# Kernel optimization log

Measured on AMD Instinct MI355X. Metric: run time of the kernel, lower is better.

## Reference

```python
import jax, jax.numpy as jnp
import numpy as np

EPS = 1e-5


def sage_conv(x, src, dst, Wl, Wr, b, n):
    # PyG SAGEConv: out_i = W_l * mean_{j in N(i)} x_j + W_r * x_i + b
    agg = jax.ops.segment_sum(x[src], dst, num_segments=n)  # [N, d]
    deg = jax.ops.segment_sum(jnp.ones_like(src, dtype=x.dtype), dst, num_segments=n)
    agg = agg / jnp.maximum(deg, 1.0)[:, None]
    return agg @ Wl + x @ Wr + b


def setup_inputs() -> dict:
    key = jax.random.key(0)
    ks = jax.random.split(key, 12)
    N, E, D_IN, D_H, D_OUT = 50000, 600000, 128, 128, 64
    x = jax.random.normal(ks[0], (N, D_IN), dtype=jnp.float32)
    edge_index = jax.random.randint(ks[1], (2, E), 0, N, dtype=jnp.int64)
    s_in = 1.0 / np.sqrt(D_IN)
    s_h = 1.0 / np.sqrt(D_H)
    return {
        "x": x,
        "edge_index": edge_index,
        "Wl0": jax.random.normal(ks[2], (D_IN, D_H), jnp.float32) * s_in,
        "Wr0": jax.random.normal(ks[3], (D_IN, D_H), jnp.float32) * s_in,
        "b0": jnp.zeros((D_H,), jnp.float32),
        "Wl1": jax.random.normal(ks[4], (D_H, D_H), jnp.float32) * s_h,
        "Wr1": jax.random.normal(ks[5], (D_H, D_H), jnp.float32) * s_h,
        "b1": jnp.zeros((D_H,), jnp.float32),
        "Wl2": jax.random.normal(ks[6], (D_H, D_OUT), jnp.float32) * s_h,
        "Wr2": jax.random.normal(ks[7], (D_H, D_OUT), jnp.float32) * s_h,
        "b2": jnp.zeros((D_OUT,), jnp.float32),
        "gamma": jnp.ones((D_H,), jnp.float32),
        "beta": jnp.zeros((D_H,), jnp.float32),
    }


def reference(x, edge_index, Wl0, Wr0, b0, Wl1, Wr1, b1, Wl2, Wr2, b2, gamma, beta):
    n = x.shape[0]
    src, dst = edge_index[0], edge_index[1]
    residual = x  # in_channels == hidden_channels -> no residual_transform
    # layer 0: conv + relu (+ dropout as identity in eval)
    h = jax.nn.relu(sage_conv(x, src, dst, Wl0, Wr0, b0, n))
    # middle layer: conv + BN(batch stats) + relu + residual
    h = sage_conv(h, src, dst, Wl1, Wr1, b1, n)
    mu = jnp.mean(h, axis=0)
    var = jnp.var(h, axis=0)  # biased, as in torch BN normalization
    h = (h - mu) * jax.lax.rsqrt(var + EPS) * gamma + beta
    h = jax.nn.relu(h) + residual
    # output layer
    h = sage_conv(h, src, dst, Wl2, Wr2, b2, n)
    return jax.nn.log_softmax(h, axis=-1)
```

## Files before the change

kernel.cpp:

```cpp
#include <hip/hip_runtime.h>
#include <hip/hip_bf16.h>


#define WS_EPS 1e-5f

typedef unsigned short ushort_t;
typedef unsigned int uint_t;
typedef ushort_t ushort8 __attribute__((ext_vector_type(8)));
typedef short short8 __attribute__((ext_vector_type(8)));
typedef float f32x4 __attribute__((ext_vector_type(4)));

__device__ __forceinline__ float bf2f(ushort_t u) {
    return __uint_as_float(((uint_t)u) << 16);
}
__device__ __forceinline__ ushort_t f2bf(float f) {
    uint_t u = __float_as_uint(f);
    u = (u + 0x7fffu + ((u >> 16) & 1u)) >> 16;
    return (ushort_t)u;
}

__global__ __launch_bounds__(256) void k_deg(const int* __restrict__ ei,
                                             int* __restrict__ deg, int E) {
    int e = blockIdx.x * 256 + threadIdx.x;
    if (e < E) atomicAdd(&deg[ei[E + e]], 1);
}

constexpr int SCHUNK = 4096;

__global__ __launch_bounds__(256) void k_scan_part(const int* __restrict__ deg,
                                                   int* __restrict__ bsum, int n) {
    int t = threadIdx.x;
    int base = blockIdx.x * SCHUNK + t * 16;
    int s = 0;
#pragma unroll
    for (int j = 0; j < 16; ++j) {
        int i = base + j;
        if (i < n) s += deg[i];
    }
#pragma unroll
    for (int d = 1; d < 64; d <<= 1) s += __shfl_xor(s, d);
    __shared__ int wt[4];
    if ((t & 63) == 0) wt[t >> 6] = s;
    __syncthreads();
    if (t == 0) bsum[blockIdx.x] = wt[0] + wt[1] + wt[2] + wt[3];
}

__global__ __launch_bounds__(64) void k_scan_bsum(const int* __restrict__ bsum,
                                                  int* __restrict__ boff,
                                                  int* __restrict__ off_n, int nb) {
    int lane = threadIdx.x;
    int carry = 0;
    for (int base = 0; base < nb; base += 64) {
        int t = base + lane;
        int v = (t < nb) ? bsum[t] : 0;
        int x = v;
#pragma unroll
        for (int d = 1; d < 64; d <<= 1) {
            int y = __shfl_up(x, d);
            if (lane >= d) x += y;
        }
        if (t < nb) boff[t] = carry + x - v;
        carry += __shfl(x, 63);
    }
    if (lane == 0) *off_n = carry;
}

__global__ __launch_bounds__(256) void k_scan_apply(const int* __restrict__ deg,
                                                    const int* __restrict__ boff,
                                                    int* __restrict__ off, int n) {
    int t = threadIdx.x;
    int lane = t & 63, wid = t >> 6;
    int base = blockIdx.x * SCHUNK + t * 16;
    int v[16];
    int s = 0;
#pragma unroll
    for (int j = 0; j < 16; ++j) {
        int i = base + j;
        v[j] = (i < n) ? deg[i] : 0;
        s += v[j];
    }
    int x = s;
#pragma unroll
    for (int d = 1; d < 64; d <<= 1) {
        int y = __shfl_up(x, d);
        if (lane >= d) x += y;
    }
    __shared__ int wtot[4];
    if (lane == 63) wtot[wid] = x;
    __syncthreads();
    int woff = 0;
    for (int wj = 0; wj < wid; ++wj) woff += wtot[wj];
    int run = boff[blockIdx.x] + woff + x - s;
#pragma unroll
    for (int j = 0; j < 16; ++j) {
        int i = base + j;
        if (i < n) off[i] = run;
        run += v[j];
    }
}

__global__ __launch_bounds__(256) void k_scatter(const int* __restrict__ ei,
                                                 const int* __restrict__ off,
                                                 int* __restrict__ cur,
                                                 int* __restrict__ csr, int E) {
    int e = blockIdx.x * 256 + threadIdx.x;
    if (e < E) {
        int d = ei[E + e];
        int s = ei[e];
        int p = atomicAdd(&cur[d], 1);
        csr[off[d] + p] = s;
    }
}

__global__ __launch_bounds__(256) void k_prep(const float* __restrict__ x,
                                              ushort_t* __restrict__ xb, int total2,
                                              int nb_cvt,
                                              const float* __restrict__ Wl0,
                                              const float* __restrict__ Wr0,
                                              const float* __restrict__ Wl1,
                                              const float* __restrict__ Wr1,
                                              const float* __restrict__ Wl2,
                                              const float* __restrict__ Wr2,
                                              ushort_t* __restrict__ wts) {
    int b = blockIdx.x;
    if (b < nb_cvt) {
        int i = b * 256 + threadIdx.x;
        if (i >= total2) return;
        float2 v = *(const float2*)&x[(size_t)i * 2];
        uint_t p = (uint_t)f2bf(v.x) | ((uint_t)f2bf(v.y) << 16);
        *(uint_t*)&xb[(size_t)i * 2] = p;
        return;
    }
    int id = (b - nb_cvt) * 256 + threadIdx.x;
    if (id >= 81920) return;
    const float* W;
    int rel, nout, base;
    if (id < 65536) {
        int m = id >> 14;
        rel = id & 16383;
        nout = 128;
        base = m << 14;
        W = (m == 0) ? Wl0 : (m == 1) ? Wr0 : (m == 2) ? Wl1 : Wr1;
    } else {
        int m = (id - 65536) >> 13;
        rel = (id - 65536) & 8191;
        nout = 64;
        base = 65536 + (m << 13);
        W = (m == 0) ? Wl2 : Wr2;
    }
    int c = rel >> 7;
    int k = rel & 127;
    wts[base + rel] = f2bf(W[(size_t)k * nout + c]);
}

template <int EPI>
__global__ __launch_bounds__(256) void k_fgemm(const ushort_t* __restrict__ X1,
                                               const ushort_t* __restrict__ W1,
                                               const ushort_t* __restrict__ X2,
                                               const ushort_t* __restrict__ W2,
                                               const float* __restrict__ bias,
                                               void* __restrict__ outv,
                                               float* __restrict__ stats, int n) {
    constexpr int NOUT = 128, BM = 128, K = 128, LDK = 136;
    constexpr int WM = 64, WN = 64, FM = 4, FN = 4;

    __shared__ ushort_t Xs[BM * LDK];
    __shared__ ushort_t Ws[NOUT * LDK];

    const int t = threadIdx.x;
    const int row0 = blockIdx.x * BM;
    const int lane = t & 63;
    const int wid = t >> 6;
    const int wr = wid >> 1, wc = wid & 1;
    const int r16 = lane & 15, kb = lane >> 4;

    f32x4 acc[FM][FN];
#pragma unroll
    for (int i = 0; i < FM; ++i)
#pragma unroll
        for (int j = 0; j < FN; ++j) acc[i][j] = (f32x4)0.f;

#pragma unroll
    for (int ph = 0; ph < 2; ++ph) {
        const ushort_t* Xp = ph ? X2 : X1;
        const ushort_t* Wp = ph ? W2 : W1;
        if (ph) __syncthreads();
#pragma unroll
        for (int u = 0; u < 8; ++u) {
            int f = u * 256 + t;
            int r = f >> 4, seg = f & 15;
            int gr = row0 + r;
            ushort8 v = (ushort8)0;
            if (gr < n) v = *(const ushort8*)&Xp[(size_t)gr * K + seg * 8];
            *(ushort8*)&Xs[r * LDK + seg * 8] = v;
        }
#pragma unroll
        for (int u = 0; u < 8; ++u) {
            int f = u * 256 + t;
            int r = f >> 4, seg = f & 15;
            *(ushort8*)&Ws[r * LDK + seg * 8] = *(const ushort8*)&Wp[(size_t)r * K + seg * 8];
        }
        __syncthreads();
#pragma unroll
        for (int ks = 0; ks < 4; ++ks) {
            short8 a[FM], b[FN];
#pragma unroll
            for (int fm = 0; fm < FM; ++fm)
                a[fm] = *(const short8*)&Xs[(wr * WM + fm * 16 + r16) * LDK + ks * 32 + kb * 8];
#pragma unroll
            for (int fn = 0; fn < FN; ++fn)
                b[fn] = *(const short8*)&Ws[(wc * WN + fn * 16 + r16) * LDK + ks * 32 + kb * 8];
#pragma unroll
            for (int fm = 0; fm < FM; ++fm)
#pragma unroll
                for (int fn = 0; fn < FN; ++fn)
                    acc[fm][fn] = __builtin_amdgcn_mfma_f32_16x16x32_bf16(a[fm], b[fn], acc[fm][fn], 0, 0, 0);
        }
    }

    if constexpr (EPI == 2) {
#pragma unroll
        for (int fm = 0; fm < FM; ++fm) {
#pragma unroll
            for (int r = 0; r < 4; ++r) {
                int row = row0 + wr * WM + fm * 16 + kb * 4 + r;
                if (row >= n) continue;
#pragma unroll
                for (int fn = 0; fn < FN; ++fn) {
                    int col = wc * WN + fn * 16 + r16;
                    float v = acc[fm][fn][r] + bias[col];
                    ((ushort_t*)outv)[(size_t)row * NOUT + col] = f2bf(fmaxf(v, 0.f));
                }
            }
        }
    } else {
        float s[FN], q[FN];
#pragma unroll
        for (int fn = 0; fn < FN; ++fn) { s[fn] = 0.f; q[fn] = 0.f; }
#pragma unroll
        for (int fm = 0; fm < FM; ++fm) {
#pragma unroll
            for (int r = 0; r < 4; ++r) {
                int row = row0 + wr * WM + fm * 16 + kb * 4 + r;
                if (row >= n) continue;
#pragma unroll
                for (int fn = 0; fn < FN; ++fn) {
                    int col = wc * WN + fn * 16 + r16;
                    float v = acc[fm][fn][r] + bias[col];
                    ((float*)outv)[(size_t)row * NOUT + col] = v;
                    s[fn] += v;
                    q[fn] += v * v;
                }
            }
        }
#pragma unroll
        for (int fn = 0; fn < FN; ++fn) {
            s[fn] += __shfl_xor(s[fn], 16);
            s[fn] += __shfl_xor(s[fn], 32);
            q[fn] += __shfl_xor(q[fn], 16);
            q[fn] += __shfl_xor(q[fn], 32);
        }
        if (kb == 0) {
#pragma unroll
            for (int fn = 0; fn < FN; ++fn) {
                int col = wc * WN + fn * 16 + r16;
                atomicAdd(&stats[col], s[fn]);
                atomicAdd(&stats[128 + col], q[fn]);
            }
        }
    }
}

template <int EPI>
__global__ __launch_bounds__(256) void k_mgemm64(const ushort_t* __restrict__ X,
                                                 const ushort_t* __restrict__ WT,
                                                 const ushort_t* __restrict__ AGG,
                                                 const float* __restrict__ bias,
                                                 void* __restrict__ outv, int n) {
    constexpr int NOUT = 64, BM = 128, K = 128, LDK = 136;
    constexpr int WM = 32, WN = 64, FM = 2, FN = 4;

    __shared__ ushort_t Xs[BM * LDK];
    __shared__ ushort_t Ws[NOUT * LDK];

    const int t = threadIdx.x;
    const int row0 = blockIdx.x * BM;

#pragma unroll
    for (int u = 0; u < 8; ++u) {
        int f = u * 256 + t;
        int r = f >> 4, seg = f & 15;
        int gr = row0 + r;
        ushort8 v = (ushort8)0;
        if (gr < n) v = *(const ushort8*)&X[(size_t)gr * K + seg * 8];
        *(ushort8*)&Xs[r * LDK + seg * 8] = v;
    }
#pragma unroll
    for (int u = 0; u < 4; ++u) {
        int f = u * 256 + t;
        int r = f >> 4, seg = f & 15;
        *(ushort8*)&Ws[r * LDK + seg * 8] = *(const ushort8*)&WT[(size_t)r * K + seg * 8];
    }
    __syncthreads();

    const int lane = t & 63;
    const int wid = t >> 6;
    const int r16 = lane & 15, kb = lane >> 4;

    f32x4 acc[FM][FN];
#pragma unroll
    for (int i = 0; i < FM; ++i)
#pragma unroll
        for (int j = 0; j < FN; ++j) acc[i][j] = (f32x4)0.f;

#pragma unroll
    for (int ks = 0; ks < 4; ++ks) {
        short8 a[FM], b[FN];
#pragma unroll
        for (int fm = 0; fm < FM; ++fm)
            a[fm] = *(const short8*)&Xs[(wid * WM + fm * 16 + r16) * LDK + ks * 32 + kb * 8];
#pragma unroll
        for (int fn = 0; fn < FN; ++fn)
            b[fn] = *(const short8*)&Ws[(fn * 16 + r16) * LDK + ks * 32 + kb * 8];
#pragma unroll
        for (int fm = 0; fm < FM; ++fm)
#pragma unroll
            for (int fn = 0; fn < FN; ++fn)
                acc[fm][fn] = __builtin_amdgcn_mfma_f32_16x16x32_bf16(a[fm], b[fn], acc[fm][fn], 0, 0, 0);
    }

    if constexpr (EPI == 3) {
        float* outp = (float*)outv;
#pragma unroll
        for (int fm = 0; fm < FM; ++fm) {
#pragma unroll
            for (int r = 0; r < 4; ++r) {
                int row = row0 + wid * WM + fm * 16 + kb * 4 + r;
                bool ok = (row < n);
                float vv[FN];
#pragma unroll
                for (int fn = 0; fn < FN; ++fn) {
                    int col = fn * 16 + r16;
                    vv[fn] = ok ? (acc[fm][fn][r] + bf2f(AGG[(size_t)row * NOUT + col]) + bias[col])
                                : 0.f;
                }
                float m = fmaxf(fmaxf(vv[0], vv[1]), fmaxf(vv[2], vv[3]));
#pragma unroll
                for (int d = 1; d < 16; d <<= 1) m = fmaxf(m, __shfl_xor(m, d));
                float e = expf(vv[0] - m) + expf(vv[1] - m) + expf(vv[2] - m) + expf(vv[3] - m);
#pragma unroll
                for (int d = 1; d < 16; d <<= 1) e += __shfl_xor(e, d);
                float lg = m + logf(e);
                if (ok) {
#pragma unroll
                    for (int fn = 0; fn < FN; ++fn)
                        outp[(size_t)row * NOUT + fn * 16 + r16] = vv[fn] - lg;
                }
            }
        }
    } else {
#pragma unroll
        for (int fm = 0; fm < FM; ++fm) {
#pragma unroll
            for (int r = 0; r < 4; ++r) {
                int row = row0 + wid * WM + fm * 16 + kb * 4 + r;
                if (row >= n) continue;
#pragma unroll
                for (int fn = 0; fn < FN; ++fn) {
                    int col = fn * 16 + r16;
                    ((ushort_t*)outv)[(size_t)row * NOUT + col] = f2bf(acc[fm][fn][r]);
                }
            }
        }
    }
}

template <int D>
__global__ __launch_bounds__(256) void k_segmean_bf(const ushort_t* __restrict__ U,
                                                    const int* __restrict__ off,
                                                    const int* __restrict__ srcs,
                                                    ushort_t* __restrict__ out,
                                                    int n) {
    int node = blockIdx.x * 8 + (threadIdx.x >> 5);
    int sub = threadIdx.x & 31;
    if (node >= n) return;
    int beg = off[node], end = off[node + 1];
    constexpr int CPL = D / 32;
    float a0 = 0.f, a1 = 0.f, a2 = 0.f, a3 = 0.f;
    int i = beg;
    for (; i + 8 <= end; i += 8) {
        int sv[8];
#pragma unroll
        for (int u = 0; u < 8; ++u) sv[u] = srcs[i + u];
#pragma unroll
        for (int u = 0; u < 8; ++u) {
            if (CPL == 4) {
                uint2 v = *(const uint2*)&U[(size_t)sv[u] * D + sub * 4];
                a0 += __uint_as_float(v.x << 16);
                a1 += __uint_as_float(v.x & 0xffff0000u);
                a2 += __uint_as_float(v.y << 16);
                a3 += __uint_as_float(v.y & 0xffff0000u);
            } else {
                uint_t v = *(const uint_t*)&U[(size_t)sv[u] * D + sub * 2];
                a0 += __uint_as_float(v << 16);
                a1 += __uint_as_float(v & 0xffff0000u);
            }
        }
    }
    for (; i + 4 <= end; i += 4) {
        int sv[4];
#pragma unroll
        for (int u = 0; u < 4; ++u) sv[u] = srcs[i + u];
#pragma unroll
        for (int u = 0; u < 4; ++u) {
            if (CPL == 4) {
                uint2 v = *(const uint2*)&U[(size_t)sv[u] * D + sub * 4];
                a0 += __uint_as_float(v.x << 16);
                a1 += __uint_as_float(v.x & 0xffff0000u);
                a2 += __uint_as_float(v.y << 16);
                a3 += __uint_as_float(v.y & 0xffff0000u);
            } else {
                uint_t v = *(const uint_t*)&U[(size_t)sv[u] * D + sub * 2];
                a0 += __uint_as_float(v << 16);
                a1 += __uint_as_float(v & 0xffff0000u);
            }
        }
    }
    for (; i < end; ++i) {
        int s = srcs[i];
        if (CPL == 4) {
            uint2 v = *(const uint2*)&U[(size_t)s * D + sub * 4];
            a0 += __uint_as_float(v.x << 16);
            a1 += __uint_as_float(v.x & 0xffff0000u);
            a2 += __uint_as_float(v.y << 16);
            a3 += __uint_as_float(v.y & 0xffff0000u);
        } else {
            uint_t v = *(const uint_t*)&U[(size_t)s * D + sub * 2];
            a0 += __uint_as_float(v << 16);
            a1 += __uint_as_float(v & 0xffff0000u);
        }
    }
    int d = end - beg;
    float inv = 1.f / (float)(d > 1 ? d : 1);
    if (CPL == 4) {
        uint2 p;
        p.x = (uint_t)f2bf(a0 * inv) | ((uint_t)f2bf(a1 * inv) << 16);
        p.y = (uint_t)f2bf(a2 * inv) | ((uint_t)f2bf(a3 * inv) << 16);
        *(uint2*)&out[(size_t)node * D + sub * 4] = p;
    } else {
        uint_t p = (uint_t)f2bf(a0 * inv) | ((uint_t)f2bf(a1 * inv) << 16);
        *(uint_t*)&out[(size_t)node * D + sub * 2] = p;
    }
}

__global__ __launch_bounds__(256) void k_bnapply(const float* __restrict__ P,
                                                 const float* __restrict__ X,
                                                 const float* __restrict__ stats,
                                                 const float* __restrict__ gamma,
                                                 const float* __restrict__ beta,
                                                 ushort_t* __restrict__ H, int n) {
    int i = blockIdx.x * 256 + threadIdx.x;
    if (i >= n * 64) return;
    int nd = i >> 6;
    int c = (i & 63) << 1;
    float inv_n = 1.f / (float)n;
    float mu0 = stats[c] * inv_n, mu1 = stats[c + 1] * inv_n;
    float v0 = stats[128 + c] * inv_n - mu0 * mu0;
    float v1 = stats[128 + c + 1] * inv_n - mu1 * mu1;
    float s0 = rsqrtf(v0 + WS_EPS) * gamma[c];
    float s1 = rsqrtf(v1 + WS_EPS) * gamma[c + 1];
    float2 p = *(const float2*)&P[(size_t)nd * 128 + c];
    float2 xr = *(const float2*)&X[(size_t)nd * 128 + c];
    float h0 = fmaxf((p.x - mu0) * s0 + beta[c], 0.f) + xr.x;
    float h1 = fmaxf((p.y - mu1) * s1 + beta[c + 1], 0.f) + xr.y;
    uint_t pk = (uint_t)f2bf(h0) | ((uint_t)f2bf(h1) << 16);
    *(uint_t*)&H[(size_t)nd * 128 + c] = pk;
}

extern "C" void kernel_launch(void* const* d_in, const int* in_sizes, int n_in,
                              void* d_out, int out_size, void* d_ws, size_t ws_size,
                              hipStream_t stream) {
    const float* x     = (const float*)d_in[0];
    const int*   ei    = (const int*)d_in[1];
    const float* Wl0   = (const float*)d_in[2];
    const float* Wr0   = (const float*)d_in[3];
    const float* b0    = (const float*)d_in[4];
    const float* Wl1   = (const float*)d_in[5];
    const float* Wr1   = (const float*)d_in[6];
    const float* b1    = (const float*)d_in[7];
    const float* Wl2   = (const float*)d_in[8];
    const float* Wr2   = (const float*)d_in[9];
    const float* b2    = (const float*)d_in[10];
    const float* gamma = (const float*)d_in[11];
    const float* beta  = (const float*)d_in[12];

    const int n = in_sizes[0] / 128;
    const int E = in_sizes[1] / 2;
    const int nb_scan = (n + SCHUNK - 1) / SCHUNK;

    char* w = (char*)d_ws;
    auto alloc = [&](size_t bytes) -> void* {
        void* p = (void*)w;
        w += (bytes + 255) & ~(size_t)255;
        return p;
    };
    int*      deg   = (int*)alloc((size_t)n * 4);
    int*      cur   = (int*)alloc((size_t)n * 4);
    float*    stats = (float*)alloc(256 * 4);
    size_t    zbytes = (size_t)((char*)w - (char*)deg);
    int*      off   = (int*)alloc(((size_t)n + 1) * 4);
    int*      csr   = (int*)alloc((size_t)E * 4);
    int*      bsum  = (int*)alloc(256 * 4);
    int*      boff  = (int*)alloc(256 * 4);
    ushort_t* wts   = (ushort_t*)alloc((size_t)81920 * 2);
    ushort_t* xb    = (ushort_t*)alloc((size_t)n * 128 * 2);
    ushort_t* H     = (ushort_t*)alloc((size_t)n * 128 * 2);
    float*    P     = (float*)alloc((size_t)n * 128 * 4);
    ushort_t* slabB = (ushort_t*)alloc((size_t)n * 128 * 2);

    ushort_t* WtL0 = wts;
    ushort_t* WtR0 = wts + 16384;
    ushort_t* WtL1 = wts + 32768;
    ushort_t* WtR1 = wts + 49152;
    ushort_t* WtL2 = wts + 65536;
    ushort_t* WtR2 = wts + 73728;

    ushort_t* M   = slabB;
    ushort_t* A64 = slabB;
    ushort_t* B64 = slabB + (size_t)n * 64;

    hipMemsetAsync(deg, 0, zbytes, stream);

    const int eb = (E + 255) / 256;
    k_deg<<<eb, 256, 0, stream>>>(ei, deg, E);
    k_scan_part<<<nb_scan, 256, 0, stream>>>(deg, bsum, n);
    k_scan_bsum<<<1, 64, 0, stream>>>(bsum, boff, off + n, nb_scan);
    k_scan_apply<<<nb_scan, 256, 0, stream>>>(deg, boff, off, n);
    k_scatter<<<eb, 256, 0, stream>>>(ei, off, cur, csr, E);

    const int nb_cvt = (n * 64 + 255) / 256;
    k_prep<<<nb_cvt + 320, 256, 0, stream>>>(x, xb, n * 64, nb_cvt,
                                             Wl0, Wr0, Wl1, Wr1, Wl2, Wr2, wts);

    const int gb = (n + 127) / 128;
    const int smb = (n + 7) / 8;

    k_segmean_bf<128><<<smb, 256, 0, stream>>>(xb, off, csr, M, n);
    k_fgemm<2><<<gb, 256, 0, stream>>>(xb, WtR0, M, WtL0, b0, H, nullptr, n);

    k_segmean_bf<128><<<smb, 256, 0, stream>>>(H, off, csr, M, n);
    k_fgemm<1><<<gb, 256, 0, stream>>>(H, WtR1, M, WtL1, b1, P, stats, n);
    k_bnapply<<<(n * 64 + 255) / 256, 256, 0, stream>>>(P, x, stats, gamma, beta, H, n);

    k_mgemm64<0><<<gb, 256, 0, stream>>>(H, WtL2, nullptr, nullptr, A64, n);
    k_segmean_bf<64><<<smb, 256, 0, stream>>>(A64, off, csr, B64, n);
    k_mgemm64<3><<<gb, 256, 0, stream>>>(H, WtR2, B64, b2, (float*)d_out, n);
}
```

Baseline: 233.4 us.

## Halve GEMM row tiles, read weights from global, prefetch second operand, block-reduce BN stats

```diff
diff --git a/kernel.cpp b/kernel.cpp
--- a/kernel.cpp
+++ b/kernel.cpp
@@ -154,18 +154,18 @@
 }
 
 template <int EPI>
-__global__ __launch_bounds__(256) void k_fgemm(const ushort_t* __restrict__ X1,
-                                               const ushort_t* __restrict__ W1,
-                                               const ushort_t* __restrict__ X2,
-                                               const ushort_t* __restrict__ W2,
-                                               const float* __restrict__ bias,
-                                               void* __restrict__ outv,
-                                               float* __restrict__ stats, int n) {
-    constexpr int NOUT = 128, BM = 128, K = 128, LDK = 136;
-    constexpr int WM = 64, WN = 64, FM = 4, FN = 4;
-
-    __shared__ ushort_t Xs[BM * LDK];
-    __shared__ ushort_t Ws[NOUT * LDK];
+__global__ __launch_bounds__(256, 4) void k_fgemm(const ushort_t* __restrict__ X1,
+                                                  const ushort_t* __restrict__ W1,
+                                                  const ushort_t* __restrict__ X2,
+                                                  const ushort_t* __restrict__ W2,
+                                                  const float* __restrict__ bias,
+                                                  void* __restrict__ outv,
+                                                  float* __restrict__ stats, int n) {
+    constexpr int NOUT = 128, K = 128, BM = 64, LDK = 136;
+    constexpr int FM = 2, FN = 4;
+
+    __shared__ ushort_t Xs[2][BM * LDK];
+    __shared__ float sred[256];
 
     const int t = threadIdx.x;
     const int row0 = blockIdx.x * BM;
@@ -173,6 +173,26 @@
     const int wid = t >> 6;
     const int wr = wid >> 1, wc = wid & 1;
     const int r16 = lane & 15, kb = lane >> 4;
+    const int tr = t >> 4, seg = t & 15;
+
+    if (EPI == 1) sred[t] = 0.f;
+
+    ushort8 g[4];
+#pragma unroll
+    for (int u = 0; u < 4; ++u) {
+        int gr = row0 + u * 16 + tr;
+        g[u] = (gr < n) ? *(const ushort8*)&X1[(size_t)gr * K + seg * 8] : (ushort8)0;
+    }
+#pragma unroll
+    for (int u = 0; u < 4; ++u)
+        *(ushort8*)&Xs[0][(u * 16 + tr) * LDK + seg * 8] = g[u];
+    __syncthreads();
+
+#pragma unroll
+    for (int u = 0; u < 4; ++u) {
+        int gr = row0 + u * 16 + tr;
+        g[u] = (gr < n) ? *(const ushort8*)&X2[(size_t)gr * K + seg * 8] : (ushort8)0;
+    }
 
     f32x4 acc[FM][FN];
 #pragma unroll
@@ -181,41 +201,40 @@
         for (int j = 0; j < FN; ++j) acc[i][j] = (f32x4)0.f;
 
 #pragma unroll
-    for (int ph = 0; ph < 2; ++ph) {
-        const ushort_t* Xp = ph ? X2 : X1;
-        const ushort_t* Wp = ph ? W2 : W1;
-        if (ph) __syncthreads();
-#pragma unroll
-        for (int u = 0; u < 8; ++u) {
-            int f = u * 256 + t;
-            int r = f >> 4, seg = f & 15;
-            int gr = row0 + r;
-            ushort8 v = (ushort8)0;
-            if (gr < n) v = *(const ushort8*)&Xp[(size_t)gr * K + seg * 8];
-            *(ushort8*)&Xs[r * LDK + seg * 8] = v;
-        }
-#pragma unroll
-        for (int u = 0; u < 8; ++u) {
-            int f = u * 256 + t;
-            int r = f >> 4, seg = f & 15;
-            *(ushort8*)&Ws[r * LDK + seg * 8] = *(const ushort8*)&Wp[(size_t)r * K + seg * 8];
-        }
-        __syncthreads();
-#pragma unroll
-        for (int ks = 0; ks < 4; ++ks) {
-            short8 a[FM], b[FN];
-#pragma unroll
-            for (int fm = 0; fm < FM; ++fm)
-                a[fm] = *(const short8*)&Xs[(wr * WM + fm * 16 + r16) * LDK + ks * 32 + kb * 8];
+    for (int ks = 0; ks < 4; ++ks) {
+        short8 a[FM], b[FN];
+#pragma unroll
+        for (int fm = 0; fm < FM; ++fm)
+            a[fm] = *(const short8*)&Xs[0][(wr * 32 + fm * 16 + r16) * LDK + ks * 32 + kb * 8];
+#pragma unroll
+        for (int fn = 0; fn < FN; ++fn)
+            b[fn] = *(const short8*)&W1[(size_t)(wc * 64 + fn * 16 + r16) * K + ks * 32 + kb * 8];
+#pragma unroll
+        for (int fm = 0; fm < FM; ++fm)
 #pragma unroll
             for (int fn = 0; fn < FN; ++fn)
-                b[fn] = *(const short8*)&Ws[(wc * WN + fn * 16 + r16) * LDK + ks * 32 + kb * 8];
-#pragma unroll
-            for (int fm = 0; fm < FM; ++fm)
-#pragma unroll
-                for (int fn = 0; fn < FN; ++fn)
-                    acc[fm][fn] = __builtin_amdgcn_mfma_f32_16x16x32_bf16(a[fm], b[fn], acc[fm][fn], 0, 0, 0);
-        }
+                acc[fm][fn] = __builtin_amdgcn_mfma_f32_16x16x32_bf16(a[fm], b[fn], acc[fm][fn], 0, 0, 0);
+    }
+
+#pragma unroll
+    for (int u = 0; u < 4; ++u)
+        *(ushort8*)&Xs[1][(u * 16 + tr) * LDK + seg * 8] = g[u];
+    __syncthreads();
+
+#pragma unroll
+    for (int ks = 0; ks < 4; ++ks) {
+        short8 a[FM], b[FN];
+#pragma unroll
+        for (int fm = 0; fm < FM; ++fm)
+            a[fm] = *(const short8*)&Xs[1][(wr * 32 + fm * 16 + r16) * LDK + ks * 32 + kb * 8];
+#pragma unroll
+        for (int fn = 0; fn < FN; ++fn)
+            b[fn] = *(const short8*)&W2[(size_t)(wc * 64 + fn * 16 + r16) * K + ks * 32 + kb * 8];
+#pragma unroll
+        for (int fm = 0; fm < FM; ++fm)
+#pragma unroll
+            for (int fn = 0; fn < FN; ++fn)
+                acc[fm][fn] = __builtin_amdgcn_mfma_f32_16x16x32_bf16(a[fm], b[fn], acc[fm][fn], 0, 0, 0);
     }
 
     if constexpr (EPI == 2) {
@@ -223,11 +242,11 @@
         for (int fm = 0; fm < FM; ++fm) {
 #pragma unroll
             for (int r = 0; r < 4; ++r) {
-                int row = row0 + wr * WM + fm * 16 + kb * 4 + r;
+                int row = row0 + wr * 32 + fm * 16 + kb * 4 + r;
                 if (row >= n) continue;
 #pragma unroll
                 for (int fn = 0; fn < FN; ++fn) {
-                    int col = wc * WN + fn * 16 + r16;
+                    int col = wc * 64 + fn * 16 + r16;
                     float v = acc[fm][fn][r] + bias[col];
                     ((ushort_t*)outv)[(size_t)row * NOUT + col] = f2bf(fmaxf(v, 0.f));
                 }
@@ -241,11 +260,11 @@
         for (int fm = 0; fm < FM; ++fm) {
 #pragma unroll
             for (int r = 0; r < 4; ++r) {
-                int row = row0 + wr * WM + fm * 16 + kb * 4 + r;
+                int row = row0 + wr * 32 + fm * 16 + kb * 4 + r;
                 if (row >= n) continue;
 #pragma unroll
                 for (int fn = 0; fn < FN; ++fn) {
-                    int col = wc * WN + fn * 16 + r16;
+                    int col = wc * 64 + fn * 16 + r16;
                     float v = acc[fm][fn][r] + bias[col];
                     ((float*)outv)[(size_t)row * NOUT + col] = v;
                     s[fn] += v;
@@ -263,113 +282,93 @@
         if (kb == 0) {
 #pragma unroll
             for (int fn = 0; fn < FN; ++fn) {
-                int col = wc * WN + fn * 16 + r16;
-                atomicAdd(&stats[col], s[fn]);
-                atomicAdd(&stats[128 + col], q[fn]);
-            }
-        }
+                int col = wc * 64 + fn * 16 + r16;
+                atomicAdd(&sred[col], s[fn]);
+                atomicAdd(&sred[128 + col], q[fn]);
+            }
+        }
+        __syncthreads();
+        atomicAdd(&stats[t], sred[t]);
     }
 }
 
 template <int EPI>
-__global__ __launch_bounds__(256) void k_mgemm64(const ushort_t* __restrict__ X,
-                                                 const ushort_t* __restrict__ WT,
-                                                 const ushort_t* __restrict__ AGG,
-                                                 const float* __restrict__ bias,
-                                                 void* __restrict__ outv, int n) {
-    constexpr int NOUT = 64, BM = 128, K = 128, LDK = 136;
-    constexpr int WM = 32, WN = 64, FM = 2, FN = 4;
+__global__ __launch_bounds__(256, 4) void k_mgemm64(const ushort_t* __restrict__ X,
+                                                    const ushort_t* __restrict__ WT,
+                                                    const ushort_t* __restrict__ AGG,
+                                                    const float* __restrict__ bias,
+                                                    void* __restrict__ outv, int n) {
+    constexpr int NOUT = 64, K = 128, BM = 64, LDK = 136;
+    constexpr int FN = 4;
 
     __shared__ ushort_t Xs[BM * LDK];
-    __shared__ ushort_t Ws[NOUT * LDK];
 
     const int t = threadIdx.x;
     const int row0 = blockIdx.x * BM;
-
-#pragma unroll
-    for (int u = 0; u < 8; ++u) {
-        int f = u * 256 + t;
-        int r = f >> 4, seg = f & 15;
-        int gr = row0 + r;
-        ushort8 v = (ushort8)0;
-        if (gr < n) v = *(const ushort8*)&X[(size_t)gr * K + seg * 8];
-        *(ushort8*)&Xs[r * LDK + seg * 8] = v;
-    }
-#pragma unroll
-    for (int u = 0; u < 4; ++u) {
-        int f = u * 256 + t;
-        int r = f >> 4, seg = f & 15;
-        *(ushort8*)&Ws[r * LDK + seg * 8] = *(const ushort8*)&WT[(size_t)r * K + seg * 8];
-    }
-    __syncthreads();
-
     const int lane = t & 63;
     const int wid = t >> 6;
     const int r16 = lane & 15, kb = lane >> 4;
-
-    f32x4 acc[FM][FN];
-#pragma unroll
-    for (int i = 0; i < FM; ++i)
-#pragma unroll
-        for (int j = 0; j < FN; ++j) acc[i][j] = (f32x4)0.f;
+    const int tr = t >> 4, seg = t & 15;
+
+#pragma unroll
+    for (int u = 0; u < 4; ++u) {
+        int gr = row0 + u * 16 + tr;
+        ushort8 v = (gr < n) ? *(const ushort8*)&X[(size_t)gr * K + seg * 8] : (ushort8)0;
+        *(ushort8*)&Xs[(u * 16 + tr) * LDK + seg * 8] = v;
+    }
+    __syncthreads();
+
+    f32x4 acc[FN];
+#pragma unroll
+    for (int j = 0; j < FN; ++j) acc[j] = (f32x4)0.f;
 
 #pragma unroll
     for (int ks = 0; ks < 4; ++ks) {
-        short8 a[FM], b[FN];
-#pragma unroll
-        for (int fm = 0; fm < FM; ++fm)
-            a[fm] = *(const short8*)&Xs[(wid * WM + fm * 16 + r16) * LDK + ks * 32 + kb * 8];
+        short8 a = *(const short8*)&Xs[(wid * 16 + r16) * LDK + ks * 32 + kb * 8];
+        short8 b[FN];
 #pragma unroll
         for (int fn = 0; fn < FN; ++fn)
-            b[fn] = *(const short8*)&Ws[(fn * 16 + r16) * LDK + ks * 32 + kb * 8];
-#pragma unroll
-        for (int fm = 0; fm < FM; ++fm)
-#pragma unroll
-            for (int fn = 0; fn < FN; ++fn)
-                acc[fm][fn] = __builtin_amdgcn_mfma_f32_16x16x32_bf16(a[fm], b[fn], acc[fm][fn], 0, 0, 0);
+            b[fn] = *(const short8*)&WT[(size_t)(fn * 16 + r16) * K + ks * 32 + kb * 8];
+#pragma unroll
+        for (int fn = 0; fn < FN; ++fn)
+            acc[fn] = __builtin_amdgcn_mfma_f32_16x16x32_bf16(a, b[fn], acc[fn], 0, 0, 0);
     }
 
     if constexpr (EPI == 3) {
         float* outp = (float*)outv;
 #pragma unroll
-        for (int fm = 0; fm < FM; ++fm) {
-#pragma unroll
-            for (int r = 0; r < 4; ++r) {
-                int row = row0 + wid * WM + fm * 16 + kb * 4 + r;
-                bool ok = (row < n);
-                float vv[FN];
-#pragma unroll
-                for (int fn = 0; fn < FN; ++fn) {
-                    int col = fn * 16 + r16;
-                    vv[fn] = ok ? (acc[fm][fn][r] + bf2f(AGG[(size_t)row * NOUT + col]) + bias[col])
-                                : 0.f;
-                }
-                float m = fmaxf(fmaxf(vv[0], vv[1]), fmaxf(vv[2], vv[3]));
-#pragma unroll
-                for (int d = 1; d < 16; d <<= 1) m = fmaxf(m, __shfl_xor(m, d));
-                float e = expf(vv[0] - m) + expf(vv[1] - m) + expf(vv[2] - m) + expf(vv[3] - m);
-#pragma unroll
-                for (int d = 1; d < 16; d <<= 1) e += __shfl_xor(e, d);
-                float lg = m + logf(e);
-                if (ok) {
-#pragma unroll
-                    for (int fn = 0; fn < FN; ++fn)
-                        outp[(size_t)row * NOUT + fn * 16 + r16] = vv[fn] - lg;
-                }
+        for (int r = 0; r < 4; ++r) {
+            int row = row0 + wid * 16 + kb * 4 + r;
+            bool ok = (row < n);
+            float vv[FN];
+#pragma unroll
+            for (int fn = 0; fn < FN; ++fn) {
+                int col = fn * 16 + r16;
+                vv[fn] = ok ? (acc[fn][r] + bf2f(AGG[(size_t)row * NOUT + col]) + bias[col])
+                            : 0.f;
+            }
+            float m = fmaxf(fmaxf(vv[0], vv[1]), fmaxf(vv[2], vv[3]));
+#pragma unroll
+            for (int d = 1; d < 16; d <<= 1) m = fmaxf(m, __shfl_xor(m, d));
+            float e = expf(vv[0] - m) + expf(vv[1] - m) + expf(vv[2] - m) + expf(vv[3] - m);
+#pragma unroll
+            for (int d = 1; d < 16; d <<= 1) e += __shfl_xor(e, d);
+            float lg = m + logf(e);
+            if (ok) {
+#pragma unroll
+                for (int fn = 0; fn < FN; ++fn)
+                    outp[(size_t)row * NOUT + fn * 16 + r16] = vv[fn] - lg;
             }
         }
     } else {
 #pragma unroll
-        for (int fm = 0; fm < FM; ++fm) {
-#pragma unroll
-            for (int r = 0; r < 4; ++r) {
-                int row = row0 + wid * WM + fm * 16 + kb * 4 + r;
-                if (row >= n) continue;
-#pragma unroll
-                for (int fn = 0; fn < FN; ++fn) {
-                    int col = fn * 16 + r16;
-                    ((ushort_t*)outv)[(size_t)row * NOUT + col] = f2bf(acc[fm][fn][r]);
-                }
+        for (int r = 0; r < 4; ++r) {
+            int row = row0 + wid * 16 + kb * 4 + r;
+            if (row >= n) continue;
+#pragma unroll
+            for (int fn = 0; fn < FN; ++fn) {
+                int col = fn * 16 + r16;
+                ((ushort_t*)outv)[(size_t)row * NOUT + col] = f2bf(acc[fn][r]);
             }
         }
     }
@@ -542,7 +541,7 @@
     k_prep<<<nb_cvt + 320, 256, 0, stream>>>(x, xb, n * 64, nb_cvt,
                                              Wl0, Wr0, Wl1, Wr1, Wl2, Wr2, wts);
 
-    const int gb = (n + 127) / 128;
+    const int gb = (n + 63) / 64;
     const int smb = (n + 7) / 8;
 
     k_segmean_bf<128><<<smb, 256, 0, stream>>>(xb, off, csr, M, n);
```

Result: slower. 255.6 us (+9.5%).
